# Optimization experiments

Hardware: AMD Instinct MI355X
Metric: run time of the kernel (lower is better)

The kernel has to match this reference:

```python
import jax, jax.numpy as jnp
import numpy as np

DELTA = 1.0
EPS = 1e-8  # torch CosineSimilarity eps


def setup_inputs() -> dict:
    key = jax.random.key(0)
    k1, k2, k3, k4 = jax.random.split(key, 4)
    N1, N2, D, C = 4096, 4096, 256, 16
    return {
        "mmd1": jax.random.normal(k1, (N1, D), dtype=jnp.float32),
        "mmd2": jax.random.normal(k2, (N2, D), dtype=jnp.float32),
        "label1": jax.random.randint(k3, (N1,), 0, C, dtype=jnp.int64),
        "label2": jax.random.randint(k4, (N2,), 0, C, dtype=jnp.int64),
    }


def reference(mmd1, mmd2, label1, label2):
    # Normalize rows with torch-style eps clamp: x / max(||x||, eps)
    n1 = mmd1 / jnp.maximum(jnp.linalg.norm(mmd1, axis=1, keepdims=True), EPS)
    n2 = mmd2 / jnp.maximum(jnp.linalg.norm(mmd2, axis=1, keepdims=True), EPS)
    cos = jnp.einsum("id,jd->ij", n1, n2)  # [N1, N2] pairwise cosine
    same = label1[:, None] == label2[None, :]  # [N1, N2] bool
    per_pair = jnp.where(same, jnp.maximum(DELTA - cos, 0.0), cos)
    return jnp.mean(per_pair)
```

## Files before the change

kernel.cpp:

```cpp
#include <hip/hip_runtime.h>
#include <cstdint>

#define N1 4096
#define N2 4096
#define DD 256
#define NCLS 16
#define EPSN 1e-8f

#define CS_BLOCKS 512
#define CS_THREADS 512

__global__ __launch_bounds__(CS_THREADS) void fused_classsum_kernel(
    const float* __restrict__ mmd1, const float* __restrict__ mmd2,
    const int* __restrict__ lab1, const int* __restrict__ lab2,
    float* __restrict__ ws_acc, float* __restrict__ out)
{
    __shared__ float part[NCLS * DD];
    __shared__ int hist[NCLS];
    __shared__ float wredS[4], wredA[4];
    __shared__ int isLast;

    float* cs1 = ws_acc;
    float* cs2 = ws_acc + NCLS * DD;
    float* cc1 = ws_acc + 2 * NCLS * DD;
    float* cc2 = cc1 + NCLS;
    float* counter = cc2 + NCLS;

    const int t = threadIdx.x;
    const int lane = t & 63, wid = t >> 6;
    const int side = blockIdx.x >> 8;
    const int lb = blockIdx.x & 255;

    #pragma unroll
    for (int s = t; s < NCLS * DD; s += CS_THREADS) part[s] = 0.0f;
    if (t < NCLS) hist[t] = 0;
    __syncthreads();

    const float* srcbase = side ? mmd2 : mmd1;
    const int* labbase = side ? lab2 : lab1;
    const int row0 = lb * 16 + wid * 2;

    #pragma unroll
    for (int rr = 0; rr < 2; ++rr) {
        int row = row0 + rr;
        const float* src = srcbase + (size_t)row * DD;
        float x0 = src[lane];
        float x1 = src[lane + 64];
        float x2 = src[lane + 128];
        float x3 = src[lane + 192];
        float ss = x0 * x0 + x1 * x1 + x2 * x2 + x3 * x3;
        #pragma unroll
        for (int off = 32; off; off >>= 1) ss += __shfl_xor(ss, off, 64);
        float sc = 1.0f / fmaxf(sqrtf(ss), EPSN);
        int cls = labbase[row];
        float* prow = &part[cls * DD];
        atomicAdd(&prow[lane],        x0 * sc);
        atomicAdd(&prow[lane + 64],   x1 * sc);
        atomicAdd(&prow[lane + 128],  x2 * sc);
        atomicAdd(&prow[lane + 192],  x3 * sc);
        if (lane == 0) atomicAdd(&hist[cls], 1);
    }
    __syncthreads();

    float* cs = side ? cs2 : cs1;
    #pragma unroll
    for (int s = t; s < NCLS * DD; s += CS_THREADS) atomicAdd(&cs[s], part[s]);
    if (t < NCLS) atomicAdd((side ? cc2 : cc1) + t, (float)hist[t]);

    __syncthreads();
    if (t == 0) {
        __threadfence();
        float old = atomicAdd(counter, 1.0f);
        isLast = (old > (float)CS_BLOCKS - 1.5f) ? 1 : 0;
    }
    __syncthreads();
    if (!isLast) return;

    float dsame = 0.0f, dall = 0.0f;
    if (t < DD) {
        float a1 = 0.0f, a2 = 0.0f;
        #pragma unroll
        for (int c = 0; c < NCLS; ++c) {
            float s1 = atomicAdd(&cs1[c * DD + t], 0.0f);
            float s2 = atomicAdd(&cs2[c * DD + t], 0.0f);
            a1 += s1; a2 += s2; dsame += s1 * s2;
        }
        dall = a1 * a2;
        #pragma unroll
        for (int off = 32; off; off >>= 1) {
            dsame += __shfl_xor(dsame, off, 64);
            dall  += __shfl_xor(dall,  off, 64);
        }
        if (lane == 0) { wredS[wid] = dsame; wredA[wid] = dall; }
    }
    __syncthreads();
    if (t == 0) {
        float Dsame = wredS[0] + wredS[1] + wredS[2] + wredS[3];
        float Dall  = wredA[0] + wredA[1] + wredA[2] + wredA[3];
        float scount = 0.0f;
        for (int c = 0; c < NCLS; ++c) {
            float c1 = atomicAdd(&cc1[c], 0.0f);
            float c2 = atomicAdd(&cc2[c], 0.0f);
            scount += c1 * c2;
        }
        out[0] = (scount + Dall - 2.0f * Dsame)
                 * (1.0f / ((float)N1 * (float)N2));
    }
}

extern "C" void kernel_launch(void* const* d_in, const int* in_sizes, int n_in,
                              void* d_out, int out_size, void* d_ws, size_t ws_size,
                              hipStream_t stream) {
    const float* mmd1 = (const float*)d_in[0];
    const float* mmd2 = (const float*)d_in[1];
    const int* lab1 = (const int*)d_in[2];
    const int* lab2 = (const int*)d_in[3];

    fused_classsum_kernel<<<CS_BLOCKS, CS_THREADS, 0, stream>>>(
        mmd1, mmd2, lab1, lab2, (float*)d_ws, (float*)d_out);
}
```

Before: 93.79 us.

## Replace global atomic class-sum accumulation with per-block partials and a reduction kernel

```diff
diff --git a/kernel.cpp b/kernel.cpp
--- a/kernel.cpp
+++ b/kernel.cpp
@@ -9,22 +9,24 @@
 
 #define CS_BLOCKS 512
 #define CS_THREADS 512
+#define SLICES 256
+#define PSTRIDE (NCLS * DD)
 
-__global__ __launch_bounds__(CS_THREADS) void fused_classsum_kernel(
+#define RED_BLOCKS 32
+#define RED_THREADS 256
+
+#define OFF_HISTS   (CS_BLOCKS * PSTRIDE)
+#define OFF_TOTALS  (OFF_HISTS + CS_BLOCKS * NCLS)
+#define OFF_CTOT    (OFF_TOTALS + 2 * PSTRIDE)
+#define OFF_COUNTER (OFF_CTOT + 2 * NCLS)
+
+__global__ __launch_bounds__(CS_THREADS) void classsum_kernel(
     const float* __restrict__ mmd1, const float* __restrict__ mmd2,
     const int* __restrict__ lab1, const int* __restrict__ lab2,
-    float* __restrict__ ws_acc, float* __restrict__ out)
+    float* __restrict__ ws)
 {
-    __shared__ float part[NCLS * DD];
+    __shared__ float part[PSTRIDE];
     __shared__ int hist[NCLS];
-    __shared__ float wredS[4], wredA[4];
-    __shared__ int isLast;
-
-    float* cs1 = ws_acc;
-    float* cs2 = ws_acc + NCLS * DD;
-    float* cc1 = ws_acc + 2 * NCLS * DD;
-    float* cc2 = cc1 + NCLS;
-    float* counter = cc2 + NCLS;
 
     const int t = threadIdx.x;
     const int lane = t & 63, wid = t >> 6;
@@ -32,7 +34,7 @@
     const int lb = blockIdx.x & 255;
 
     #pragma unroll
-    for (int s = t; s < NCLS * DD; s += CS_THREADS) part[s] = 0.0f;
+    for (int s = t; s < PSTRIDE; s += CS_THREADS) part[s] = 0.0f;
     if (t < NCLS) hist[t] = 0;
     __syncthreads();
 
@@ -62,45 +64,86 @@
     }
     __syncthreads();
 
-    float* cs = side ? cs2 : cs1;
+    float* dst = ws + (size_t)blockIdx.x * PSTRIDE;
     #pragma unroll
-    for (int s = t; s < NCLS * DD; s += CS_THREADS) atomicAdd(&cs[s], part[s]);
-    if (t < NCLS) atomicAdd((side ? cc2 : cc1) + t, (float)hist[t]);
+    for (int s = t; s < PSTRIDE; s += CS_THREADS) dst[s] = part[s];
+    if (t < NCLS) ws[OFF_HISTS + blockIdx.x * NCLS + t] = (float)hist[t];
+}
+
+__global__ __launch_bounds__(RED_THREADS) void reduce_finalize_kernel(
+    float* __restrict__ ws, float* __restrict__ out)
+{
+    __shared__ float wredS[4], wredA[4];
+    __shared__ int isLast;
+
+    const int g = blockIdx.x;
+    const int side = g >> 4;
+    const int ebase = (g & 15) * RED_THREADS;
+    const int t = threadIdx.x;
+    const int lane = t & 63, wid = t >> 6;
+    const int e = ebase + t;
+
+    const float* src = ws + (size_t)(side * SLICES) * PSTRIDE + e;
+    float a[16];
+    #pragma unroll
+    for (int i = 0; i < 16; ++i) a[i] = 0.0f;
+    for (int b = 0; b < SLICES; b += 16) {
+        #pragma unroll
+        for (int i = 0; i < 16; ++i)
+            a[i] += src[(size_t)(b + i) * PSTRIDE];
+    }
+    float tot = 0.0f;
+    #pragma unroll
+    for (int i = 0; i < 16; ++i) tot += a[i];
+    ws[OFF_TOTALS + side * PSTRIDE + e] = tot;
+
+    if ((g & 15) == 0) {
+        int c = t & 15, chunk = t >> 4;
+        float cc = 0.0f;
+        #pragma unroll
+        for (int i = 0; i < 16; ++i)
+            cc += ws[OFF_HISTS + (size_t)(side * SLICES + chunk * 16 + i) * NCLS + c];
+        __shared__ float chist[NCLS];
+        if (t < NCLS) chist[t] = 0.0f;
+        __syncthreads();
+        atomicAdd(&chist[c], cc);
+        __syncthreads();
+        if (t < NCLS) ws[OFF_CTOT + side * NCLS + t] = chist[t];
+    }
 
     __syncthreads();
     if (t == 0) {
         __threadfence();
-        float old = atomicAdd(counter, 1.0f);
-        isLast = (old > (float)CS_BLOCKS - 1.5f) ? 1 : 0;
+        float old = atomicAdd(&ws[OFF_COUNTER], 1.0f);
+        isLast = (old > (float)RED_BLOCKS - 1.5f) ? 1 : 0;
     }
     __syncthreads();
     if (!isLast) return;
 
-    float dsame = 0.0f, dall = 0.0f;
-    if (t < DD) {
-        float a1 = 0.0f, a2 = 0.0f;
-        #pragma unroll
-        for (int c = 0; c < NCLS; ++c) {
-            float s1 = atomicAdd(&cs1[c * DD + t], 0.0f);
-            float s2 = atomicAdd(&cs2[c * DD + t], 0.0f);
-            a1 += s1; a2 += s2; dsame += s1 * s2;
-        }
-        dall = a1 * a2;
-        #pragma unroll
-        for (int off = 32; off; off >>= 1) {
-            dsame += __shfl_xor(dsame, off, 64);
-            dall  += __shfl_xor(dall,  off, 64);
-        }
-        if (lane == 0) { wredS[wid] = dsame; wredA[wid] = dall; }
+    float* cs1 = ws + OFF_TOTALS;
+    float* cs2 = ws + OFF_TOTALS + PSTRIDE;
+    float a1 = 0.0f, a2 = 0.0f, dsame = 0.0f;
+    #pragma unroll
+    for (int c = 0; c < NCLS; ++c) {
+        float s1 = atomicAdd(&cs1[c * DD + t], 0.0f);
+        float s2 = atomicAdd(&cs2[c * DD + t], 0.0f);
+        a1 += s1; a2 += s2; dsame += s1 * s2;
     }
+    float dall = a1 * a2;
+    #pragma unroll
+    for (int off = 32; off; off >>= 1) {
+        dsame += __shfl_xor(dsame, off, 64);
+        dall  += __shfl_xor(dall,  off, 64);
+    }
+    if (lane == 0) { wredS[wid] = dsame; wredA[wid] = dall; }
     __syncthreads();
     if (t == 0) {
         float Dsame = wredS[0] + wredS[1] + wredS[2] + wredS[3];
         float Dall  = wredA[0] + wredA[1] + wredA[2] + wredA[3];
         float scount = 0.0f;
         for (int c = 0; c < NCLS; ++c) {
-            float c1 = atomicAdd(&cc1[c], 0.0f);
-            float c2 = atomicAdd(&cc2[c], 0.0f);
+            float c1 = atomicAdd(&ws[OFF_CTOT + c], 0.0f);
+            float c2 = atomicAdd(&ws[OFF_CTOT + NCLS + c], 0.0f);
             scount += c1 * c2;
         }
         out[0] = (scount + Dall - 2.0f * Dsame)
@@ -116,6 +159,9 @@
     const int* lab1 = (const int*)d_in[2];
     const int* lab2 = (const int*)d_in[3];
 
-    fused_classsum_kernel<<<CS_BLOCKS, CS_THREADS, 0, stream>>>(
-        mmd1, mmd2, lab1, lab2, (float*)d_ws, (float*)d_out);
+    float* ws = (float*)d_ws;
+    float* out = (float*)d_out;
+
+    classsum_kernel<<<CS_BLOCKS, CS_THREADS, 0, stream>>>(mmd1, mmd2, lab1, lab2, ws);
+    reduce_finalize_kernel<<<RED_BLOCKS, RED_THREADS, 0, stream>>>(ws, out);
 }
```

Result: slower. 113.4 us (+20.9%).
